# Optimization experiments

Hardware: AMD Instinct MI355X
Metric: run time of the kernel (lower is better)

The kernel has to match this reference:

```python
import jax, jax.numpy as jnp
import numpy as np

B, L, C, D = 8, 8192, 256, 256


def setup_inputs() -> dict:
    key = jax.random.key(0)
    ks = jax.random.split(key, 13)
    bound = 1.0 / np.sqrt(C)

    def W(k):
        return jax.random.uniform(k, (C, D), jnp.float32, -bound, bound)

    def b(k):
        return jax.random.uniform(k, (D,), jnp.float32, -bound, bound)

    return {
        "xs": jax.random.normal(ks[0], (B, L, C), jnp.float32),
        # forward-direction params
        "Wh1": W(ks[1]), "bh1": b(ks[2]),
        "Wz1": W(ks[3]), "bz1": b(ks[4]),
        "Ws1": W(ks[5]), "bs1": b(ks[6]),
        "h01": jnp.zeros((1, 1, D), jnp.float32),
        # backward-direction params
        "Wh_1": W(ks[7]), "bh_1": b(ks[8]),
        "Wz_1": W(ks[9]), "bz_1": b(ks[10]),
        "Ws_1": W(ks[11]), "bs_1": b(ks[12]),
        "h0_1": jnp.zeros((1, 1, D), jnp.float32),
    }


def _gru_scan(z, h_tilde, h0):
    """h[t] = z[t]*h_tilde[t] + (1-z[t])*h[t-1], h[-1]=h0. Parallel over time
    via associative scan on the affine maps h -> a*h + b."""
    a = 1.0 - z            # [B, L, D]
    b = z * h_tilde        # [B, L, D]

    def combine(c1, c2):
        a1, b1 = c1
        a2, b2 = c2
        return a1 * a2, a2 * b1 + b2

    A, Bc = jax.lax.associative_scan(combine, (a, b), axis=1)
    return Bc + A * h0     # broadcast h0 [1,1,D]


def reference(xs, Wh1, bh1, Wz1, bz1, Ws1, bs1, h01,
              Wh_1, bh_1, Wz_1, bz_1, Ws_1, bs_1, h0_1):
    sig = jax.nn.sigmoid
    # forward direction
    hf = _gru_scan(sig(xs @ Wz1 + bz1), xs @ Wh1 + bh1, h01) * sig(xs @ Ws1 + bs1)
    # backward direction: reverse time, scan, reverse back
    zr = sig(xs @ Wz_1 + bz_1)
    hr = xs @ Wh_1 + bh_1
    hb = _gru_scan(zr[:, ::-1], hr[:, ::-1], h0_1)[:, ::-1] * sig(xs @ Ws_1 + bs_1)
    return hf + hb
```

## Files before the change

kernel.cpp:

```cpp
#include <hip/hip_runtime.h>
#include <hip/hip_bf16.h>

typedef unsigned short u16;

#define BDIM 8
#define LDIM 8192
#define KDIM 256
#define DDIM 256
#define MTOT 65536
#define NDIM 1536
#define TCH  32
#define NCH  256


typedef float floatx4 __attribute__((ext_vector_type(4)));
typedef short bf16x8 __attribute__((ext_vector_type(8)));

__device__ __forceinline__ u16 f2bf(float f) {
  union { __hip_bfloat16 h; u16 u; } c;
  c.h = __float2bfloat16(f);
  return c.u;
}
__device__ __forceinline__ float bf2f(u16 u) {
  union { unsigned int i; float f; } c;
  c.i = ((unsigned int)u) << 16;
  return c.f;
}
__device__ __forceinline__ float sigmoidf_fast(float x) {
  return __builtin_amdgcn_rcpf(1.0f + __expf(-x));
}
__device__ __forceinline__ void gll16(const u16* g, u16* l) {
  __builtin_amdgcn_global_load_lds((const __attribute__((address_space(1))) void*)g,
                                   (__attribute__((address_space(3))) void*)l, 16, 0, 0);
}

__global__ void prep_weights(const float* __restrict__ Wh1, const float* __restrict__ Wz1,
                             const float* __restrict__ Ws1, const float* __restrict__ Wh_1,
                             const float* __restrict__ Wz_1, const float* __restrict__ Ws_1,
                             const float* __restrict__ bh1, const float* __restrict__ bz1,
                             const float* __restrict__ bs1, const float* __restrict__ bh_1,
                             const float* __restrict__ bz_1, const float* __restrict__ bs_1,
                             u16* __restrict__ WcatT, float* __restrict__ bcat) {
  const int n = blockIdx.x;
  const int k = threadIdx.x;
  const int dir = n / 768, r = n % 768;
  int d; const float* W; const float* bb;
  if (r < 512) {
    d = r >> 1;
    if (r & 1) { W = dir ? Wz_1 : Wz1; bb = dir ? bz_1 : bz1; }
    else       { W = dir ? Wh_1 : Wh1; bb = dir ? bh_1 : bh1; }
  } else {
    d = r - 512;
    W = dir ? Ws_1 : Ws1; bb = dir ? bs_1 : bs1;
  }
  WcatT[(size_t)n * KDIM + k] = f2bf(W[k * DDIM + d]);
  if (k == 0) bcat[n] = bb[d];
}

__global__ void convert_xs(const float* __restrict__ xs, u16* __restrict__ Abf) {
  size_t i = ((size_t)blockIdx.x * 256 + threadIdx.x) * 8;
  const float4* s = (const float4*)(xs + i);
  float4 f0 = s[0], f1 = s[1];
  union { u16 u[8]; uint4 v; } t;
  t.u[0] = f2bf(f0.x); t.u[1] = f2bf(f0.y); t.u[2] = f2bf(f0.z); t.u[3] = f2bf(f0.w);
  t.u[4] = f2bf(f1.x); t.u[5] = f2bf(f1.y); t.u[6] = f2bf(f1.z); t.u[7] = f2bf(f1.w);
  *(uint4*)(Abf + i) = t.v;
}

__global__ __launch_bounds__(256) void gemm_kernel(const u16* __restrict__ Abf,
                                                   const u16* __restrict__ WcatT,
                                                   const float* __restrict__ bcat,
                                                   u16* __restrict__ G) {
  __shared__ __align__(16) u16 As[4096];
  __shared__ __align__(16) u16 Bs[4096];
  const int tid = threadIdx.x;
  const int lane = tid & 63, wave = tid >> 6;
  const int wm = wave >> 1, wn = wave & 1;
  const int q = lane >> 4, r = lane & 15;

  const int xcd = blockIdx.x & 7;
  const int li  = blockIdx.x >> 3;
  const int mt  = xcd * 64 + li / 12;
  const int nt  = li % 12;
  const int m0 = mt * 128, n0 = nt * 128;

  const int bi0 = wave * 128 + lane;
  const int bi1 = bi0 + 64;
  const u16* gA0 = Abf   + (size_t)(m0 + (bi0 >> 2)) * KDIM + (bi0 & 3) * 8;
  const u16* gA1 = Abf   + (size_t)(m0 + (bi1 >> 2)) * KDIM + (bi1 & 3) * 8;
  const u16* gB0 = WcatT + (size_t)(n0 + (bi0 >> 2)) * KDIM + (bi0 & 3) * 8;
  const u16* gB1 = WcatT + (size_t)(n0 + (bi1 >> 2)) * KDIM + (bi1 & 3) * 8;
  u16* lA0 = As + wave * 1024;
  u16* lA1 = As + wave * 1024 + 512;
  u16* lB0 = Bs + wave * 1024;
  u16* lB1 = Bs + wave * 1024 + 512;

  floatx4 acc[4][4];
  floatx4 z4 = {0.f, 0.f, 0.f, 0.f};
#pragma unroll
  for (int i = 0; i < 4; i++)
#pragma unroll
    for (int j = 0; j < 4; j++) acc[i][j] = z4;

  for (int k0 = 0; k0 < KDIM; k0 += 32) {
    gll16(gA0 + k0, lA0);
    gll16(gA1 + k0, lA1);
    gll16(gB0 + k0, lB0);
    gll16(gB1 + k0, lB1);
    __syncthreads();
    bf16x8 af[4], bv[4];
#pragma unroll
    for (int i = 0; i < 4; i++)
      af[i] = *(const bf16x8*)(As + ((wm * 64 + i * 16 + r) * 4 + q) * 8);
#pragma unroll
    for (int j = 0; j < 4; j++)
      bv[j] = *(const bf16x8*)(Bs + ((wn * 64 + j * 16 + r) * 4 + q) * 8);
#pragma unroll
    for (int i = 0; i < 4; i++)
#pragma unroll
      for (int j = 0; j < 4; j++)
        acc[i][j] = __builtin_amdgcn_mfma_f32_16x16x32_bf16(af[i], bv[j], acc[i][j], 0, 0, 0);
    __syncthreads();
  }

  float bvals[4];
#pragma unroll
  for (int j = 0; j < 4; j++) bvals[j] = bcat[n0 + wn * 64 + j * 16 + r];
#pragma unroll
  for (int i = 0; i < 4; i++) {
#pragma unroll
    for (int reg = 0; reg < 4; reg++) {
      size_t grow = (size_t)(m0 + wm * 64 + i * 16 + q * 4 + reg);
      u16* dst = G + grow * NDIM + n0 + wn * 64 + r;
#pragma unroll
      for (int j = 0; j < 4; j++)
        dst[j * 16] = f2bf(acc[i][j][reg] + bvals[j]);
    }
  }
}

__global__ __launch_bounds__(256) void scan_phaseA(const u16* __restrict__ G,
                                                   float* __restrict__ Acc,
                                                   float* __restrict__ Bcc) {
  const int slot = threadIdx.x >> 6, lane = threadIdx.x & 63;
  const int u = blockIdx.x * 4 + slot;
  const int c = u & 255, b = (u >> 8) & 7, dir = u >> 11;
  const u16* p0 = G + (size_t)b * LDIM * NDIM + dir * 768 + lane * 8;
  float h[4], P[4];
#pragma unroll
  for (int e = 0; e < 4; ++e) { h[e] = 0.f; P[e] = 1.f; }
#pragma unroll 4
  for (int i = 0; i < TCH; ++i) {
    const int t = dir ? (c * TCH + (TCH - 1 - i)) : (c * TCH + i);
    uint4 hz = *(const uint4*)(p0 + (size_t)t * NDIM);
    const u16* q = (const u16*)&hz;
#pragma unroll
    for (int e = 0; e < 4; ++e) {
      float z = sigmoidf_fast(bf2f(q[2 * e + 1]));
      float a = 1.f - z;
      h[e] = fmaf(a, h[e], z * bf2f(q[2 * e]));
      P[e] *= a;
    }
  }
  float4 v;
  v.x = P[0]; v.y = P[1]; v.z = P[2]; v.w = P[3];
  *(float4*)(Acc + (size_t)u * 256 + lane * 4) = v;
  v.x = h[0]; v.y = h[1]; v.z = h[2]; v.w = h[3];
  *(float4*)(Bcc + (size_t)u * 256 + lane * 4) = v;
}

__global__ void scan_phaseB(const float* __restrict__ Acc, const float* __restrict__ Bcc,
                            const float* __restrict__ h01, const float* __restrict__ h0_1,
                            float* __restrict__ Pref) {
  const int d = threadIdx.x, b = blockIdx.x, dir = blockIdx.y;
  float h = dir ? h0_1[d] : h01[d];
  const size_t ubase = ((size_t)dir * BDIM + b) * NCH;
  if (dir == 0) {
    for (int c0 = 0; c0 < NCH; c0 += 8) {
      float a[8], bb[8];
#pragma unroll
      for (int j = 0; j < 8; ++j) {
        size_t idx = (ubase + c0 + j) * DDIM + d;
        a[j] = Acc[idx]; bb[j] = Bcc[idx];
      }
#pragma unroll
      for (int j = 0; j < 8; ++j) {
        Pref[(ubase + c0 + j) * DDIM + d] = h;
        h = fmaf(a[j], h, bb[j]);
      }
    }
  } else {
    for (int c0 = NCH - 1; c0 >= 0; c0 -= 8) {
      float a[8], bb[8];
#pragma unroll
      for (int j = 0; j < 8; ++j) {
        size_t idx = (ubase + c0 - j) * DDIM + d;
        a[j] = Acc[idx]; bb[j] = Bcc[idx];
      }
#pragma unroll
      for (int j = 0; j < 8; ++j) {
        Pref[(ubase + c0 - j) * DDIM + d] = h;
        h = fmaf(a[j], h, bb[j]);
      }
    }
  }
}

__global__ __launch_bounds__(256) void scan_phaseC_fwd(const u16* __restrict__ G,
                                                       const float* __restrict__ Pref,
                                                       float* __restrict__ out) {
  const int slot = threadIdx.x >> 6, lane = threadIdx.x & 63;
  const int u = blockIdx.x * 4 + slot;
  const int c = u & 255, b = u >> 8;
  float4 p0 = *(const float4*)(Pref + (size_t)u * 256 + lane * 4);
  float h[4] = {p0.x, p0.y, p0.z, p0.w};
  const u16* ghz = G + (size_t)b * LDIM * NDIM + lane * 8;
  const u16* gs  = G + (size_t)b * LDIM * NDIM + 512 + lane * 4;
  float* o0 = out + (size_t)b * LDIM * DDIM + lane * 4;
#pragma unroll 4
  for (int i = 0; i < TCH; ++i) {
    const int t = c * TCH + i;
    uint4 hz = *(const uint4*)(ghz + (size_t)t * NDIM);
    uint2 sv = *(const uint2*)(gs + (size_t)t * NDIM);
    const u16* q = (const u16*)&hz;
    const u16* sq = (const u16*)&sv;
    float4 v;
    float* o = (float*)&v;
#pragma unroll
    for (int e = 0; e < 4; ++e) {
      float z = sigmoidf_fast(bf2f(q[2 * e + 1]));
      h[e] = fmaf(1.f - z, h[e], z * bf2f(q[2 * e]));
      o[e] = h[e] * sigmoidf_fast(bf2f(sq[e]));
    }
    *(float4*)(o0 + (size_t)t * DDIM) = v;
  }
}

__global__ __launch_bounds__(256) void scan_phaseC_bwd(const u16* __restrict__ G,
                                                       const float* __restrict__ Pref,
                                                       float* __restrict__ out) {
  const int slot = threadIdx.x >> 6, lane = threadIdx.x & 63;
  const int u = blockIdx.x * 4 + slot;
  const int c = u & 255, b = u >> 8;
  float4 p0 = *(const float4*)(Pref + (size_t)(2048 + u) * 256 + lane * 4);
  float h[4] = {p0.x, p0.y, p0.z, p0.w};
  const u16* ghz = G + (size_t)b * LDIM * NDIM + 768 + lane * 8;
  const u16* gs  = G + (size_t)b * LDIM * NDIM + 1280 + lane * 4;
  float* o0 = out + (size_t)b * LDIM * DDIM + lane * 4;
#pragma unroll 4
  for (int i = 0; i < TCH; ++i) {
    const int t = c * TCH + (TCH - 1 - i);
    uint4 hz = *(const uint4*)(ghz + (size_t)t * NDIM);
    uint2 sv = *(const uint2*)(gs + (size_t)t * NDIM);
    const u16* q = (const u16*)&hz;
    const u16* sq = (const u16*)&sv;
    float* op = o0 + (size_t)t * DDIM;
    float4 cur = *(const float4*)op;
    float* o = (float*)&cur;
#pragma unroll
    for (int e = 0; e < 4; ++e) {
      float z = sigmoidf_fast(bf2f(q[2 * e + 1]));
      h[e] = fmaf(1.f - z, h[e], z * bf2f(q[2 * e]));
      o[e] += h[e] * sigmoidf_fast(bf2f(sq[e]));
    }
    *(float4*)op = cur;
  }
}

extern "C" void kernel_launch(void* const* d_in, const int* in_sizes, int n_in,
                              void* d_out, int out_size, void* d_ws, size_t ws_size,
                              hipStream_t stream) {
  const float* xs   = (const float*)d_in[0];
  const float* Wh1  = (const float*)d_in[1];
  const float* bh1  = (const float*)d_in[2];
  const float* Wz1  = (const float*)d_in[3];
  const float* bz1  = (const float*)d_in[4];
  const float* Ws1  = (const float*)d_in[5];
  const float* bs1  = (const float*)d_in[6];
  const float* h01  = (const float*)d_in[7];
  const float* Wh_1 = (const float*)d_in[8];
  const float* bh_1 = (const float*)d_in[9];
  const float* Wz_1 = (const float*)d_in[10];
  const float* bz_1 = (const float*)d_in[11];
  const float* Ws_1 = (const float*)d_in[12];
  const float* bs_1 = (const float*)d_in[13];
  const float* h0_1 = (const float*)d_in[14];
  float* out = (float*)d_out;

  char* ws = (char*)d_ws;
  u16* WcatT = (u16*)ws;   ws += (size_t)NDIM * KDIM * 2;
  float* bcat = (float*)ws; ws += (size_t)NDIM * 4;
  u16* Abf = (u16*)ws;     ws += (size_t)MTOT * KDIM * 2;
  u16* G = (u16*)ws;       ws += (size_t)MTOT * NDIM * 2;
  float* Acc  = (float*)Abf;
  float* Bcc  = Acc + (size_t)2 * BDIM * NCH * DDIM;
  float* Pref = Bcc + (size_t)2 * BDIM * NCH * DDIM;
  if ((size_t)(ws - (char*)d_ws) > ws_size) return;

  prep_weights<<<dim3(NDIM), dim3(KDIM), 0, stream>>>(
      Wh1, Wz1, Ws1, Wh_1, Wz_1, Ws_1, bh1, bz1, bs1, bh_1, bz_1, bs_1, WcatT, bcat);
  convert_xs<<<dim3(MTOT * KDIM / (256 * 8)), dim3(256), 0, stream>>>(xs, Abf);
  gemm_kernel<<<dim3(6144), dim3(256), 0, stream>>>(Abf, WcatT, bcat, G);
  scan_phaseA<<<dim3(1024), dim3(256), 0, stream>>>(G, Acc, Bcc);
  scan_phaseB<<<dim3(BDIM, 2), dim3(DDIM), 0, stream>>>(Acc, Bcc, h01, h0_1, Pref);
  scan_phaseC_fwd<<<dim3(512), dim3(256), 0, stream>>>(G, Pref, out);
  scan_phaseC_bwd<<<dim3(512), dim3(256), 0, stream>>>(G, Pref, out);
}
```

Before: 326.6 us.

## Fuse bidirectional scan output into one kernel and deepen GEMM K-step

The GEMM now stages a 64-wide K slice per iteration, doubling LDS tiles and halving the barrier count. Scan phase A splits each chunk across two waves, each handling half the channels, so twice as many waves run. The forward and backward phase-C kernels are merged: per chunk, the backward waves write their outputs to shared memory and the forward waves add them, so the read-modify-write of the output buffer in global memory goes away. The cost is more LDS per block (32 KB in the scan, 32 KB in the GEMM) and a block-wide barrier that leaves the forward waves idle while the backward pass runs.

```diff
diff --git a/kernel.cpp b/kernel.cpp
--- a/kernel.cpp
+++ b/kernel.cpp
@@ -71,8 +71,8 @@
                                                    const u16* __restrict__ WcatT,
                                                    const float* __restrict__ bcat,
                                                    u16* __restrict__ G) {
-  __shared__ __align__(16) u16 As[4096];
-  __shared__ __align__(16) u16 Bs[4096];
+  __shared__ __align__(16) u16 As[8192];
+  __shared__ __align__(16) u16 Bs[8192];
   const int tid = threadIdx.x;
   const int lane = tid & 63, wave = tid >> 6;
   const int wm = wave >> 1, wn = wave & 1;
@@ -84,16 +84,15 @@
   const int nt  = li % 12;
   const int m0 = mt * 128, n0 = nt * 128;
 
-  const int bi0 = wave * 128 + lane;
-  const int bi1 = bi0 + 64;
-  const u16* gA0 = Abf   + (size_t)(m0 + (bi0 >> 2)) * KDIM + (bi0 & 3) * 8;
-  const u16* gA1 = Abf   + (size_t)(m0 + (bi1 >> 2)) * KDIM + (bi1 & 3) * 8;
-  const u16* gB0 = WcatT + (size_t)(n0 + (bi0 >> 2)) * KDIM + (bi0 & 3) * 8;
-  const u16* gB1 = WcatT + (size_t)(n0 + (bi1 >> 2)) * KDIM + (bi1 & 3) * 8;
-  u16* lA0 = As + wave * 1024;
-  u16* lA1 = As + wave * 1024 + 512;
-  u16* lB0 = Bs + wave * 1024;
-  u16* lB1 = Bs + wave * 1024 + 512;
+  const u16* gA[4]; const u16* gB[4]; u16* lA[4]; u16* lB[4];
+#pragma unroll
+  for (int j = 0; j < 4; j++) {
+    const int bi = wave * 256 + j * 64 + lane;
+    gA[j] = Abf   + (size_t)(m0 + (bi >> 3)) * KDIM + (bi & 7) * 8;
+    gB[j] = WcatT + (size_t)(n0 + (bi >> 3)) * KDIM + (bi & 7) * 8;
+    lA[j] = As + bi * 8;
+    lB[j] = Bs + bi * 8;
+  }
 
   floatx4 acc[4][4];
   floatx4 z4 = {0.f, 0.f, 0.f, 0.f};
@@ -102,24 +101,25 @@
 #pragma unroll
     for (int j = 0; j < 4; j++) acc[i][j] = z4;
 
-  for (int k0 = 0; k0 < KDIM; k0 += 32) {
-    gll16(gA0 + k0, lA0);
-    gll16(gA1 + k0, lA1);
-    gll16(gB0 + k0, lB0);
-    gll16(gB1 + k0, lB1);
+  for (int k0 = 0; k0 < KDIM; k0 += 64) {
+#pragma unroll
+    for (int j = 0; j < 4; j++) { gll16(gA[j] + k0, lA[j]); gll16(gB[j] + k0, lB[j]); }
     __syncthreads();
-    bf16x8 af[4], bv[4];
-#pragma unroll
-    for (int i = 0; i < 4; i++)
-      af[i] = *(const bf16x8*)(As + ((wm * 64 + i * 16 + r) * 4 + q) * 8);
-#pragma unroll
-    for (int j = 0; j < 4; j++)
-      bv[j] = *(const bf16x8*)(Bs + ((wn * 64 + j * 16 + r) * 4 + q) * 8);
-#pragma unroll
-    for (int i = 0; i < 4; i++)
+#pragma unroll
+    for (int kk = 0; kk < 2; kk++) {
+      bf16x8 af[4], bv[4];
+#pragma unroll
+      for (int i = 0; i < 4; i++)
+        af[i] = *(const bf16x8*)(As + ((wm * 64 + i * 16 + r) * 8 + kk * 4 + q) * 8);
 #pragma unroll
       for (int j = 0; j < 4; j++)
-        acc[i][j] = __builtin_amdgcn_mfma_f32_16x16x32_bf16(af[i], bv[j], acc[i][j], 0, 0, 0);
+        bv[j] = *(const bf16x8*)(Bs + ((wn * 64 + j * 16 + r) * 8 + kk * 4 + q) * 8);
+#pragma unroll
+      for (int i = 0; i < 4; i++)
+#pragma unroll
+        for (int j = 0; j < 4; j++)
+          acc[i][j] = __builtin_amdgcn_mfma_f32_16x16x32_bf16(af[i], bv[j], acc[i][j], 0, 0, 0);
+    }
     __syncthreads();
   }
 
@@ -143,30 +143,29 @@
                                                    float* __restrict__ Acc,
                                                    float* __restrict__ Bcc) {
   const int slot = threadIdx.x >> 6, lane = threadIdx.x & 63;
-  const int u = blockIdx.x * 4 + slot;
+  const int w = blockIdx.x * 4 + slot;
+  const int u = w >> 1, half = w & 1;
   const int c = u & 255, b = (u >> 8) & 7, dir = u >> 11;
-  const u16* p0 = G + (size_t)b * LDIM * NDIM + dir * 768 + lane * 8;
-  float h[4], P[4];
-#pragma unroll
-  for (int e = 0; e < 4; ++e) { h[e] = 0.f; P[e] = 1.f; }
+  const int d0 = half * 128 + lane * 2;
+  const u16* p0 = G + (size_t)b * LDIM * NDIM + dir * 768 + d0 * 2;
+  float h0 = 0.f, h1 = 0.f, P0 = 1.f, P1 = 1.f;
 #pragma unroll 4
   for (int i = 0; i < TCH; ++i) {
     const int t = dir ? (c * TCH + (TCH - 1 - i)) : (c * TCH + i);
-    uint4 hz = *(const uint4*)(p0 + (size_t)t * NDIM);
+    uint2 hz = *(const uint2*)(p0 + (size_t)t * NDIM);
     const u16* q = (const u16*)&hz;
-#pragma unroll
-    for (int e = 0; e < 4; ++e) {
-      float z = sigmoidf_fast(bf2f(q[2 * e + 1]));
-      float a = 1.f - z;
-      h[e] = fmaf(a, h[e], z * bf2f(q[2 * e]));
-      P[e] *= a;
-    }
-  }
-  float4 v;
-  v.x = P[0]; v.y = P[1]; v.z = P[2]; v.w = P[3];
-  *(float4*)(Acc + (size_t)u * 256 + lane * 4) = v;
-  v.x = h[0]; v.y = h[1]; v.z = h[2]; v.w = h[3];
-  *(float4*)(Bcc + (size_t)u * 256 + lane * 4) = v;
+    float z0 = sigmoidf_fast(bf2f(q[1]));
+    float z1 = sigmoidf_fast(bf2f(q[3]));
+    float a0 = 1.f - z0, a1 = 1.f - z1;
+    h0 = fmaf(a0, h0, z0 * bf2f(q[0]));
+    h1 = fmaf(a1, h1, z1 * bf2f(q[2]));
+    P0 *= a0; P1 *= a1;
+  }
+  float2 v;
+  v.x = P0; v.y = P1;
+  *(float2*)(Acc + (size_t)u * 256 + d0) = v;
+  v.x = h0; v.y = h1;
+  *(float2*)(Bcc + (size_t)u * 256 + d0) = v;
 }
 
 __global__ void scan_phaseB(const float* __restrict__ Acc, const float* __restrict__ Bcc,
@@ -206,64 +205,58 @@
   }
 }
 
-__global__ __launch_bounds__(256) void scan_phaseC_fwd(const u16* __restrict__ G,
-                                                       const float* __restrict__ Pref,
-                                                       float* __restrict__ out) {
-  const int slot = threadIdx.x >> 6, lane = threadIdx.x & 63;
-  const int u = blockIdx.x * 4 + slot;
-  const int c = u & 255, b = u >> 8;
-  float4 p0 = *(const float4*)(Pref + (size_t)u * 256 + lane * 4);
-  float h[4] = {p0.x, p0.y, p0.z, p0.w};
-  const u16* ghz = G + (size_t)b * LDIM * NDIM + lane * 8;
-  const u16* gs  = G + (size_t)b * LDIM * NDIM + 512 + lane * 4;
-  float* o0 = out + (size_t)b * LDIM * DDIM + lane * 4;
+__global__ __launch_bounds__(256) void scan_phaseC(const u16* __restrict__ G,
+                                                   const float* __restrict__ Pref,
+                                                   float* __restrict__ out) {
+  __shared__ float obuf[TCH * 256];
+  const int c = blockIdx.x & 255, b = blockIdx.x >> 8;
+  const int wave = threadIdx.x >> 6, lane = threadIdx.x & 63;
+  const int dir = wave >> 1, half = wave & 1;
+  const int d0 = half * 128 + lane * 2;
+  const int u = dir * 2048 + b * 256 + c;
+  float h0 = Pref[(size_t)u * 256 + d0];
+  float h1 = Pref[(size_t)u * 256 + d0 + 1];
+  const u16* ghz = G + (size_t)b * LDIM * NDIM + dir * 768 + d0 * 2;
+  const u16* gs  = G + (size_t)b * LDIM * NDIM + dir * 768 + 512 + d0;
+
+  if (dir == 1) {
 #pragma unroll 4
-  for (int i = 0; i < TCH; ++i) {
-    const int t = c * TCH + i;
-    uint4 hz = *(const uint4*)(ghz + (size_t)t * NDIM);
-    uint2 sv = *(const uint2*)(gs + (size_t)t * NDIM);
-    const u16* q = (const u16*)&hz;
-    const u16* sq = (const u16*)&sv;
-    float4 v;
-    float* o = (float*)&v;
-#pragma unroll
-    for (int e = 0; e < 4; ++e) {
-      float z = sigmoidf_fast(bf2f(q[2 * e + 1]));
-      h[e] = fmaf(1.f - z, h[e], z * bf2f(q[2 * e]));
-      o[e] = h[e] * sigmoidf_fast(bf2f(sq[e]));
-    }
-    *(float4*)(o0 + (size_t)t * DDIM) = v;
-  }
-}
-
-__global__ __launch_bounds__(256) void scan_phaseC_bwd(const u16* __restrict__ G,
-                                                       const float* __restrict__ Pref,
-                                                       float* __restrict__ out) {
-  const int slot = threadIdx.x >> 6, lane = threadIdx.x & 63;
-  const int u = blockIdx.x * 4 + slot;
-  const int c = u & 255, b = u >> 8;
-  float4 p0 = *(const float4*)(Pref + (size_t)(2048 + u) * 256 + lane * 4);
-  float h[4] = {p0.x, p0.y, p0.z, p0.w};
-  const u16* ghz = G + (size_t)b * LDIM * NDIM + 768 + lane * 8;
-  const u16* gs  = G + (size_t)b * LDIM * NDIM + 1280 + lane * 4;
-  float* o0 = out + (size_t)b * LDIM * DDIM + lane * 4;
+    for (int i = 0; i < TCH; ++i) {
+      const int tl = TCH - 1 - i;
+      const int t = c * TCH + tl;
+      uint2 hz = *(const uint2*)(ghz + (size_t)t * NDIM);
+      unsigned int sv = *(const unsigned int*)(gs + (size_t)t * NDIM);
+      const u16* q = (const u16*)&hz;
+      const u16* sq = (const u16*)&sv;
+      float z0 = sigmoidf_fast(bf2f(q[1]));
+      float z1 = sigmoidf_fast(bf2f(q[3]));
+      h0 = fmaf(1.f - z0, h0, z0 * bf2f(q[0]));
+      h1 = fmaf(1.f - z1, h1, z1 * bf2f(q[2]));
+      float2 o;
+      o.x = h0 * sigmoidf_fast(bf2f(sq[0]));
+      o.y = h1 * sigmoidf_fast(bf2f(sq[1]));
+      *(float2*)(obuf + tl * 256 + d0) = o;
+    }
+  }
+  __syncthreads();
+  if (dir == 0) {
 #pragma unroll 4
-  for (int i = 0; i < TCH; ++i) {
-    const int t = c * TCH + (TCH - 1 - i);
-    uint4 hz = *(const uint4*)(ghz + (size_t)t * NDIM);
-    uint2 sv = *(const uint2*)(gs + (size_t)t * NDIM);
-    const u16* q = (const u16*)&hz;
-    const u16* sq = (const u16*)&sv;
-    float* op = o0 + (size_t)t * DDIM;
-    float4 cur = *(const float4*)op;
-    float* o = (float*)&cur;
-#pragma unroll
-    for (int e = 0; e < 4; ++e) {
-      float z = sigmoidf_fast(bf2f(q[2 * e + 1]));
-      h[e] = fmaf(1.f - z, h[e], z * bf2f(q[2 * e]));
-      o[e] += h[e] * sigmoidf_fast(bf2f(sq[e]));
-    }
-    *(float4*)op = cur;
+    for (int i = 0; i < TCH; ++i) {
+      const int t = c * TCH + i;
+      uint2 hz = *(const uint2*)(ghz + (size_t)t * NDIM);
+      unsigned int sv = *(const unsigned int*)(gs + (size_t)t * NDIM);
+      const u16* q = (const u16*)&hz;
+      const u16* sq = (const u16*)&sv;
+      float z0 = sigmoidf_fast(bf2f(q[1]));
+      float z1 = sigmoidf_fast(bf2f(q[3]));
+      h0 = fmaf(1.f - z0, h0, z0 * bf2f(q[0]));
+      h1 = fmaf(1.f - z1, h1, z1 * bf2f(q[2]));
+      float2 bb = *(const float2*)(obuf + i * 256 + d0);
+      float2 o;
+      o.x = fmaf(h0, sigmoidf_fast(bf2f(sq[0])), bb.x);
+      o.y = fmaf(h1, sigmoidf_fast(bf2f(sq[1])), bb.y);
+      *(float2*)(out + ((size_t)b * LDIM + t) * DDIM + d0) = o;
+    }
   }
 }
 
@@ -301,8 +294,7 @@
       Wh1, Wz1, Ws1, Wh_1, Wz_1, Ws_1, bh1, bz1, bs1, bh_1, bz_1, bs_1, WcatT, bcat);
   convert_xs<<<dim3(MTOT * KDIM / (256 * 8)), dim3(256), 0, stream>>>(xs, Abf);
   gemm_kernel<<<dim3(6144), dim3(256), 0, stream>>>(Abf, WcatT, bcat, G);
-  scan_phaseA<<<dim3(1024), dim3(256), 0, stream>>>(G, Acc, Bcc);
+  scan_phaseA<<<dim3(2048), dim3(256), 0, stream>>>(G, Acc, Bcc);
   scan_phaseB<<<dim3(BDIM, 2), dim3(DDIM), 0, stream>>>(Acc, Bcc, h01, h0_1, Pref);
-  scan_phaseC_fwd<<<dim3(512), dim3(256), 0, stream>>>(G, Pref, out);
-  scan_phaseC_bwd<<<dim3(512), dim3(256), 0, stream>>>(G, Pref, out);
-}
+  scan_phaseC<<<dim3(2048), dim3(256), 0, stream>>>(G, Pref, out);
+}
```

After: 299.2 us. 8.4% less time.
